# Kernel optimization log

Hardware: AMD Instinct MI355X
Metric: run time of the kernel (lower is better)

The kernel has to match this reference:

```python
import jax, jax.numpy as jnp
import numpy as np

EPS = 1e-5


def conv2d(x, w, b, pad):
    # x: [B,C,H,W], w: [O,I,kh,kw]
    out = jax.lax.conv_general_dilated(
        x, w, window_strides=(1, 1), padding=[(pad, pad), (pad, pad)],
        dimension_numbers=('NCHW', 'OIHW', 'NCHW'))
    return out + b[None, :, None, None]


def bilinear_gather(xf, py, px, H, W):
    # xf: [B,C,H*W]; py,px: [B,H,W] float sampling positions
    # zero padding outside the image (torchvision deform_conv2d semantics)
    y0 = jnp.floor(py)
    x0 = jnp.floor(px)
    wy = py - y0
    wx = px - x0
    y0i = y0.astype(jnp.int32)
    x0i = x0.astype(jnp.int32)
    B, C = xf.shape[0], xf.shape[1]
    acc = jnp.zeros((B, C, H, W), xf.dtype)
    for dy, wyv in ((0, 1.0 - wy), (1, wy)):
        for dx, wxv in ((0, 1.0 - wx), (1, wx)):
            yi = y0i + dy
            xi = x0i + dx
            valid = ((yi >= 0) & (yi < H) & (xi >= 0) & (xi < W)).astype(xf.dtype)
            idx = jnp.clip(yi, 0, H - 1) * W + jnp.clip(xi, 0, W - 1)  # [B,H,W]
            g = jnp.take_along_axis(xf, idx.reshape(B, 1, H * W), axis=2)
            g = g.reshape(B, C, H, W)
            acc = acc + g * (wyv * wxv * valid)[:, None]
    return acc


def deform_conv2d(x, offset, w, b, k):
    # x: [B,C,H,W]; offset: [B,2*k*k,H,W] ((dy,dx) pairs per kernel tap)
    B, C, H, W = x.shape
    pad = k // 2
    gy = jnp.arange(H, dtype=x.dtype)[None, :, None]
    gx = jnp.arange(W, dtype=x.dtype)[None, None, :]
    xf = x.reshape(B, C, H * W)
    out = jnp.zeros((B, w.shape[0], H, W), x.dtype)
    for i in range(k):
        for j in range(k):
            kk = i * k + j
            py = gy + (i - pad) + offset[:, 2 * kk]
            px = gx + (j - pad) + offset[:, 2 * kk + 1]
            samp = bilinear_gather(xf, py, px, H, W)  # [B,C,H,W]
            out = out + jnp.einsum('bchw,oc->bohw', samp, w[:, :, i, j])
    return out + b[None, :, None, None]


def setup_inputs() -> dict:
    key = jax.random.key(0)
    ks = jax.random.split(key, 16)
    B, C, H, W = 4, 64, 192, 192
    k = 3
    hid = max(1, C // 16)
    d = {}
    d['x'] = jax.random.normal(ks[0], (B, C, H, W), jnp.float32)
    # offset-prediction conv (3x3, pad 1) -> 2*k*k channels
    d['off_w'] = jax.random.normal(ks[1], (2 * k * k, C, 3, 3), jnp.float32) * 0.02
    d['off_b'] = jax.random.normal(ks[2], (2 * k * k,), jnp.float32) * 0.02
    # deformable conv weights (C->C, kxk)
    d['dw'] = jax.random.normal(ks[3], (C, C, k, k), jnp.float32) * 0.05
    d['db'] = jax.random.normal(ks[4], (C,), jnp.float32) * 0.05
    # BatchNorm (eval: running stats)
    d['bn_gamma'] = jnp.ones((C,), jnp.float32) + 0.1 * jax.random.normal(ks[5], (C,), jnp.float32)
    d['bn_beta'] = 0.1 * jax.random.normal(ks[6], (C,), jnp.float32)
    d['bn_mean'] = 0.1 * jax.random.normal(ks[7], (C,), jnp.float32)
    d['bn_var'] = jnp.ones((C,), jnp.float32)
    # channel attention: 1x1 squeeze / excite
    d['ca_w1'] = jax.random.normal(ks[8], (hid, C, 1, 1), jnp.float32) * 0.1
    d['ca_b1'] = jnp.zeros((hid,), jnp.float32)
    d['ca_w2'] = jax.random.normal(ks[9], (C, hid, 1, 1), jnp.float32) * 0.1
    d['ca_b2'] = jnp.zeros((C,), jnp.float32)
    # spatial attention: 7x7 conv -> 1 channel
    d['sa_w'] = jax.random.normal(ks[10], (1, C, 7, 7), jnp.float32) * 0.02
    d['sa_b'] = jnp.zeros((1,), jnp.float32)
    return d


def reference(x, off_w, off_b, dw, db, bn_gamma, bn_beta, bn_mean, bn_var,
              ca_w1, ca_b1, ca_w2, ca_b2, sa_w, sa_b):
    k = 3
    # extract: DeformableConv2d + BatchNorm2d
    offset = conv2d(x, off_w, off_b, pad=1)
    h = deform_conv2d(x, offset, dw, db, k)
    inv = jax.lax.rsqrt(bn_var + EPS)
    h = (h - bn_mean[None, :, None, None]) * (bn_gamma * inv)[None, :, None, None] \
        + bn_beta[None, :, None, None]
    # channel attention
    pooled = jnp.mean(h, axis=(2, 3), keepdims=True)  # [B,C,1,1]
    cw = conv2d(pooled, ca_w1, ca_b1, pad=0)
    cw = jax.nn.relu(cw)
    cw = conv2d(cw, ca_w2, ca_b2, pad=0)
    cw = jax.nn.sigmoid(cw)
    h = h * cw
    # spatial attention (7x7 conv, pad 3)
    sw = jax.nn.sigmoid(conv2d(h, sa_w, sa_b, pad=3))  # [B,1,H,W]
    h = h * sw
    return h
```

## Files before the change

kernel.cpp:

```cpp
#include <hip/hip_runtime.h>
#include <hip/hip_fp16.h>

#define H_  192
#define W_  192
#define HW  36864
#define B_  4

typedef __attribute__((ext_vector_type(8))) short short8;
typedef __attribute__((ext_vector_type(4))) float f32x4;
typedef __attribute__((ext_vector_type(4))) unsigned int u32x4;
typedef unsigned short ushort_t;
typedef unsigned int uint_t;

__device__ __forceinline__ ushort_t f2h(float v) {
    __half h = __float2half(v);
    ushort_t s;
    __builtin_memcpy(&s, &h, 2);
    return s;
}
__device__ __forceinline__ float h2f(ushort_t s) {
    __half h;
    __builtin_memcpy(&h, &s, 2);
    return __half2float(h);
}
__device__ __forceinline__ __half2 u2h2(uint_t u) {
    __half2 h;
    __builtin_memcpy(&h, &u, 4);
    return h;
}
__device__ __forceinline__ uint_t h22u(__half2 h) {
    uint_t u;
    __builtin_memcpy(&u, &h, 4);
    return u;
}
__device__ __forceinline__ short8 zero8() {
    u32x4 z = {0u, 0u, 0u, 0u};
    return __builtin_bit_cast(short8, z);
}

__device__ __forceinline__ void glds16(const ushort_t* src, void* lds_base) {
    __builtin_amdgcn_global_load_lds(
        (const __attribute__((address_space(1))) void*)src,
        (__attribute__((address_space(3))) void*)lds_base, 16, 0, 0);
}

__global__ void prep_kernel(const float* __restrict__ dw, const float* __restrict__ db,
                            const float* __restrict__ g, const float* __restrict__ be,
                            const float* __restrict__ mu, const float* __restrict__ var,
                            const float* __restrict__ ow,
                            ushort_t* __restrict__ w_bf, ushort_t* __restrict__ w_off,
                            float* __restrict__ scale, float* __restrict__ shift) {
    int idx = blockIdx.x * 256 + threadIdx.x;
    if (idx < 36864) {
        int tap = idx >> 12, o = (idx >> 6) & 63, c = idx & 63;
        w_bf[idx] = f2h(dw[(o * 64 + c) * 9 + tap]);
    }
    int idx2 = idx - 36864;
    if (idx2 >= 0 && idx2 < 18432) {
        int tap = idx2 >> 11, o = (idx2 >> 6) & 31, c = idx2 & 63;
        w_off[idx2] = (o < 18) ? f2h(ow[(o * 64 + c) * 9 + tap]) : (ushort_t)0;
    }
    if (idx < 64) {
        float s = g[idx] * rsqrtf(var[idx] + 1e-5f);
        scale[idx] = s;
        shift[idx] = (db[idx] - mu[idx]) * s + be[idx];
    }
}

__global__ __launch_bounds__(256) void transpose_kernel(const float* __restrict__ x,
                                                        ushort_t* __restrict__ x_t) {
    __shared__ uint_t tlds[256 * 33];
    int tid = threadIdx.x;
    int b = blockIdx.x / 144;
    int p0 = (blockIdx.x % 144) * 256;
    ushort_t* ts = (ushort_t*)tlds;
    for (int c = 0; c < 64; ++c) {
        float v = x[((size_t)(b * 64 + c)) * HW + p0 + tid];
        ts[tid * 66 + c] = f2h(v);
    }
    __syncthreads();
#pragma unroll
    for (int j = 0; j < 8; ++j) {
        int chunk = j * 256 + tid;
        int pl = chunk >> 3, s = chunk & 7;
        int bd = pl * 33 + s * 4;
        u32x4 v = {tlds[bd], tlds[bd + 1], tlds[bd + 2], tlds[bd + 3]};
        ((u32x4*)x_t)[(size_t)(b * HW + p0) * 8 + chunk] = v;
    }
}

__device__ __forceinline__ u32x4 prd(const ushort_t* patch, int q, int slot) {
    return *(const u32x4*)((const char*)patch + q * 128 + ((slot ^ (q & 7)) << 4));
}

__device__ __forceinline__ bool corner_setup2(float ody, float odx,
                                              int ybase, int xbase, int ytop, int xleft,
                                              int* q, int* g, float* w) {
    float py = (float)ybase + ody;
    float px = (float)xbase + odx;
    float fy = floorf(py), fx = floorf(px);
    int y0 = (int)fy, x0 = (int)fx;
    float wy = py - fy, wx = px - fx;
    int y0c = min(max(y0, 0), H_ - 1), y1c = min(max(y0 + 1, 0), H_ - 1);
    int x0c = min(max(x0, 0), W_ - 1), x1c = min(max(x0 + 1, 0), W_ - 1);
    float vy0 = (y0 >= 0 && y0 < H_) ? 1.f : 0.f;
    float vy1 = (y0 + 1 >= 0 && y0 + 1 < H_) ? 1.f : 0.f;
    float vx0 = (x0 >= 0 && x0 < W_) ? 1.f : 0.f;
    float vx1 = (x0 + 1 >= 0 && x0 + 1 < W_) ? 1.f : 0.f;
    w[0] = (1.f - wy) * (1.f - wx) * vy0 * vx0;
    w[1] = (1.f - wy) * wx * vy0 * vx1;
    w[2] = wy * (1.f - wx) * vy1 * vx0;
    w[3] = wy * wx * vy1 * vx1;
    g[0] = (y0c * W_ + x0c) * 64; g[1] = (y0c * W_ + x1c) * 64;
    g[2] = (y1c * W_ + x0c) * 64; g[3] = (y1c * W_ + x1c) * 64;
    int iy0 = y0c - ytop, iy1 = y1c - ytop;
    int ix0 = x0c - xleft, ix1 = x1c - xleft;
    q[0] = iy0 * 56 + ix0; q[1] = iy0 * 56 + ix1;
    q[2] = iy1 * 56 + ix0; q[3] = iy1 * 56 + ix1;
    return ((unsigned)iy0 <= 11u) & ((unsigned)iy1 <= 11u) &
           ((unsigned)ix0 <= 55u) & ((unsigned)ix1 <= 55u);
}

__device__ __forceinline__ short8 interp_f16(const u32x4* buf, const __half2* w2) {
    short8 r;
#pragma unroll
    for (int q = 0; q < 4; ++q) {
        __half2 acc = __hmul2(u2h2(buf[0][q]), w2[0]);
        acc = __hfma2(u2h2(buf[1][q]), w2[1], acc);
        acc = __hfma2(u2h2(buf[2][q]), w2[2], acc);
        acc = __hfma2(u2h2(buf[3][q]), w2[3], acc);
        ((uint_t*)&r)[q] = h22u(acc);
    }
    return r;
}

__global__ __launch_bounds__(576, 2) void deform_fused_kernel(
    const ushort_t* __restrict__ x_t, const ushort_t* __restrict__ w_off,
    const float* __restrict__ ob, const ushort_t* __restrict__ w_bf,
    const float* __restrict__ scale_g, const float* __restrict__ shift_g,
    float* __restrict__ out) {
    __shared__ __align__(16) ushort_t patch[672 * 64];

    int tid = threadIdx.x;
    int lane = tid & 63, w = tid >> 6;
    int tile = (blockIdx.x & 7) * 64 + (blockIdx.x >> 3);
    int b = tile / 128;
    int rem = tile % 128;
    int y0 = (rem >> 2) * 6;
    int x0 = (rem & 3) * 48;
    int ytop = y0 - 3, xleft = x0 - 4;

    int ln = lane & 15, kg = lane >> 4;
    int locA = w * 32 + ln, locB = locA + 16;
    int rowA = locA / 48, colA = locA - rowA * 48;
    int rowB = locB / 48, colB = locB - rowB * 48;
    int yA = y0 + rowA, xA = x0 + colA;
    int yB = y0 + rowB, xB = x0 + colB;
    const ushort_t* xt_b = x_t + (size_t)b * (HW * 64);

    {
        char* pbase = (char*)patch;
#pragma unroll
        for (int t = 0; t < 10; ++t) {
            if (t * 576 + w * 64 < 5376) {
                int g = t * 576 + tid;
                int q = g >> 3, sp = g & 7;
                int i = q / 56, j = q - i * 56;
                int pr = min(max(ytop + i, 0), H_ - 1);
                int pc = min(max(xleft + j, 0), W_ - 1);
                int s = sp ^ (q & 7);
                glds16(xt_b + (pr * W_ + pc) * 64 + s * 8,
                       pbase + (size_t)(t * 576 + w * 64) * 16);
            }
        }
    }
    asm volatile("s_waitcnt vmcnt(0)" ::: "memory");
    __syncthreads();

    f32x4 ao[2][2];
#pragma unroll
    for (int i = 0; i < 2; ++i)
#pragma unroll
        for (int j = 0; j < 2; ++j) ao[i][j] = (f32x4){0.f, 0.f, 0.f, 0.f};

    for (int tap = 0; tap < 9; ++tap) {
        int ti = tap / 3 - 1, tj = tap % 3 - 1;
        bool vA = ((unsigned)(yA + ti) < (unsigned)H_) && ((unsigned)(xA + tj) < (unsigned)W_);
        bool vB = ((unsigned)(yB + ti) < (unsigned)H_) && ((unsigned)(xB + tj) < (unsigned)W_);
        int qA = (rowA + 3 + ti) * 56 + (colA + 4 + tj);
        int qB = (rowB + 3 + ti) * 56 + (colB + 4 + tj);
        const ushort_t* wt = w_off + tap * 2048;
#pragma unroll
        for (int ks = 0; ks < 2; ++ks) {
            int ch = ks * 32 + kg * 8;
            int slot = kg + ks * 4;
            short8 a0 = *(const short8*)(wt + ln * 64 + ch);
            short8 a1 = *(const short8*)(wt + (16 + ln) * 64 + ch);
            short8 bA = vA ? __builtin_bit_cast(short8, prd(patch, qA, slot)) : zero8();
            short8 bB = vB ? __builtin_bit_cast(short8, prd(patch, qB, slot)) : zero8();
            ao[0][0] = __builtin_amdgcn_mfma_f32_16x16x32_f16(a0, bA, ao[0][0], 0, 0, 0);
            ao[0][1] = __builtin_amdgcn_mfma_f32_16x16x32_f16(a0, bB, ao[0][1], 0, 0, 0);
            ao[1][0] = __builtin_amdgcn_mfma_f32_16x16x32_f16(a1, bA, ao[1][0], 0, 0, 0);
            ao[1][1] = __builtin_amdgcn_mfma_f32_16x16x32_f16(a1, bB, ao[1][1], 0, 0, 0);
        }
    }

    float offA[18], offB[18];
#pragma unroll
    for (int m = 0; m < 18; ++m) {
        int src = (((m >> 2) & 3) << 4) | ln;
        float bias = ob[m];
        offA[m] = __shfl(ao[m >> 4][0][m & 3], src, 64) + bias;
        offB[m] = __shfl(ao[m >> 4][1][m & 3], src, 64) + bias;
    }

    f32x4 acc[4][2];
#pragma unroll
    for (int mt = 0; mt < 4; ++mt)
#pragma unroll
        for (int nt = 0; nt < 2; ++nt) acc[mt][nt] = (f32x4){0.f, 0.f, 0.f, 0.f};

#pragma unroll
    for (int tap = 0; tap < 9; ++tap) {
        int ti = tap / 3 - 1, tj = tap % 3 - 1;
        int qA[4], qB[4], gA[4], gB[4];
        float wA[4], wB[4];
        bool inA = corner_setup2(offA[2 * tap], offA[2 * tap + 1],
                                 yA + ti, xA + tj, ytop, xleft, qA, gA, wA);
        bool inB = corner_setup2(offB[2 * tap], offB[2 * tap + 1],
                                 yB + ti, xB + tj, ytop, xleft, qB, gB, wB);
        __half2 wA2[4], wB2[4];
#pragma unroll
        for (int c = 0; c < 4; ++c) {
            wA2[c] = __float2half2_rn(wA[c]);
            wB2[c] = __float2half2_rn(wB[c]);
        }
        const ushort_t* wt = w_bf + tap * 4096;
#pragma unroll
        for (int ks = 0; ks < 2; ++ks) {
            int ch = ks * 32 + kg * 8;
            int slot = kg + ks * 4;
            u32x4 cA[4], cB[4];
            if (__builtin_expect(inA, 1)) {
#pragma unroll
                for (int c = 0; c < 4; ++c) cA[c] = prd(patch, qA[c], slot);
            } else {
#pragma unroll
                for (int c = 0; c < 4; ++c) cA[c] = *(const u32x4*)(xt_b + gA[c] + ch);
            }
            if (__builtin_expect(inB, 1)) {
#pragma unroll
                for (int c = 0; c < 4; ++c) cB[c] = prd(patch, qB[c], slot);
            } else {
#pragma unroll
                for (int c = 0; c < 4; ++c) cB[c] = *(const u32x4*)(xt_b + gB[c] + ch);
            }
            short8 fA = interp_f16(cA, wA2);
            short8 fB = interp_f16(cB, wB2);
            short8 a0 = *(const short8*)(wt + (0 + ln) * 64 + ch);
            short8 a1 = *(const short8*)(wt + (16 + ln) * 64 + ch);
            short8 a2 = *(const short8*)(wt + (32 + ln) * 64 + ch);
            short8 a3 = *(const short8*)(wt + (48 + ln) * 64 + ch);
            acc[0][0] = __builtin_amdgcn_mfma_f32_16x16x32_f16(a0, fA, acc[0][0], 0, 0, 0);
            acc[0][1] = __builtin_amdgcn_mfma_f32_16x16x32_f16(a0, fB, acc[0][1], 0, 0, 0);
            acc[1][0] = __builtin_amdgcn_mfma_f32_16x16x32_f16(a1, fA, acc[1][0], 0, 0, 0);
            acc[1][1] = __builtin_amdgcn_mfma_f32_16x16x32_f16(a1, fB, acc[1][1], 0, 0, 0);
            acc[2][0] = __builtin_amdgcn_mfma_f32_16x16x32_f16(a2, fA, acc[2][0], 0, 0, 0);
            acc[2][1] = __builtin_amdgcn_mfma_f32_16x16x32_f16(a2, fB, acc[2][1], 0, 0, 0);
            acc[3][0] = __builtin_amdgcn_mfma_f32_16x16x32_f16(a3, fA, acc[3][0], 0, 0, 0);
            acc[3][1] = __builtin_amdgcn_mfma_f32_16x16x32_f16(a3, fB, acc[3][1], 0, 0, 0);
        }
    }

    int pixA = yA * W_ + xA;
    int pixB = yB * W_ + xB;
#pragma unroll
    for (int mt = 0; mt < 4; ++mt) {
#pragma unroll
        for (int r = 0; r < 4; ++r) {
            int m = mt * 16 + kg * 4 + r;
            float sc = scale_g[m], sh = shift_g[m];
            size_t obase = (size_t)(b * 64 + m) * HW;
            out[obase + pixA] = acc[mt][0][r] * sc + sh;
            out[obase + pixB] = acc[mt][1][r] * sc + sh;
        }
    }
}

__global__ __launch_bounds__(256) void pool_kernel(const float* __restrict__ h,
                                                   float* __restrict__ pooled) {
    __shared__ float red[4];
    int tid = threadIdx.x;
    const float* src = h + (size_t)blockIdx.x * HW;
    float s = 0.f;
#pragma unroll 4
    for (int i = tid * 4; i < HW; i += 1024) {
        float4 v = *(const float4*)(src + i);
        s += v.x + v.y + v.z + v.w;
    }
#pragma unroll
    for (int d = 1; d < 64; d <<= 1) s += __shfl_xor(s, d, 64);
    if ((tid & 63) == 0) red[tid >> 6] = s;
    __syncthreads();
    if (tid == 0)
        pooled[blockIdx.x] = (red[0] + red[1] + red[2] + red[3]) * (1.0f / (float)HW);
}

__global__ void ca_kernel(const float* __restrict__ pooled_g,
                          const float* __restrict__ w1, const float* __restrict__ b1,
                          const float* __restrict__ w2, const float* __restrict__ b2,
                          const float* __restrict__ saw, float* __restrict__ cw,
                          ushort_t* __restrict__ we_bf) {
    __shared__ float pooled[256];
    __shared__ float t1[16];
    int t = threadIdx.x;
    int b = t >> 6, o = t & 63;
    pooled[t] = pooled_g[t];
    __syncthreads();
    if (t < 16) {
        int bb = t >> 2, hh = t & 3;
        float a = b1[hh];
        for (int c = 0; c < 64; ++c) a += pooled[bb * 64 + c] * w1[hh * 64 + c];
        t1[t] = fmaxf(a, 0.f);
    }
    __syncthreads();
    float a = b2[o];
#pragma unroll
    for (int h2 = 0; h2 < 4; ++h2) a += t1[b * 4 + h2] * w2[o * 4 + h2];
    float cwv = 1.f / (1.f + __expf(-a));
    cw[t] = cwv;
    for (int tap = 0; tap < 64; ++tap) {
        float v = (tap < 49) ? cwv * saw[o * 49 + tap] : 0.f;
        we_bf[(b * 64 + tap) * 64 + o] = f2h(v);
    }
}

__global__ __launch_bounds__(256) void tap_gemm_kernel(
    const float* __restrict__ h, const ushort_t* __restrict__ we_bf,
    ushort_t* __restrict__ u) {
    int tid = threadIdx.x;
    int b = blockIdx.y;
    int p0 = blockIdx.x * 128;
    int wid = tid >> 6, lane = tid & 63, ln = lane & 15, kg = lane >> 4;
    int pA = p0 + wid * 32 + ln, pB = pA + 16;
    const float* hb = h + (size_t)b * 64 * HW;
    const ushort_t* wt = we_bf + b * 4096;

    f32x4 acc[4][2];
#pragma unroll
    for (int mt = 0; mt < 4; ++mt)
#pragma unroll
        for (int nt = 0; nt < 2; ++nt) acc[mt][nt] = (f32x4){0.f, 0.f, 0.f, 0.f};

#pragma unroll
    for (int ks = 0; ks < 2; ++ks) {
        int ch = ks * 32 + kg * 8;
        short8 fA, fB;
#pragma unroll
        for (int q = 0; q < 8; ++q) {
            fA[q] = (short)f2h(hb[(size_t)(ch + q) * HW + pA]);
            fB[q] = (short)f2h(hb[(size_t)(ch + q) * HW + pB]);
        }
        short8 a0 = *(const short8*)(wt + (0 + ln) * 64 + ch);
        short8 a1 = *(const short8*)(wt + (16 + ln) * 64 + ch);
        short8 a2 = *(const short8*)(wt + (32 + ln) * 64 + ch);
        short8 a3 = *(const short8*)(wt + (48 + ln) * 64 + ch);
        acc[0][0] = __builtin_amdgcn_mfma_f32_16x16x32_f16(a0, fA, acc[0][0], 0, 0, 0);
        acc[0][1] = __builtin_amdgcn_mfma_f32_16x16x32_f16(a0, fB, acc[0][1], 0, 0, 0);
        acc[1][0] = __builtin_amdgcn_mfma_f32_16x16x32_f16(a1, fA, acc[1][0], 0, 0, 0);
        acc[1][1] = __builtin_amdgcn_mfma_f32_16x16x32_f16(a1, fB, acc[1][1], 0, 0, 0);
        acc[2][0] = __builtin_amdgcn_mfma_f32_16x16x32_f16(a2, fA, acc[2][0], 0, 0, 0);
        acc[2][1] = __builtin_amdgcn_mfma_f32_16x16x32_f16(a2, fB, acc[2][1], 0, 0, 0);
        acc[3][0] = __builtin_amdgcn_mfma_f32_16x16x32_f16(a3, fA, acc[3][0], 0, 0, 0);
        acc[3][1] = __builtin_amdgcn_mfma_f32_16x16x32_f16(a3, fB, acc[3][1], 0, 0, 0);
    }
#pragma unroll
    for (int mt = 0; mt < 4; ++mt)
#pragma unroll
        for (int r = 0; r < 4; ++r) {
            int m = mt * 16 + kg * 4 + r;
            if (m < 49) {
                ushort_t* up = u + (size_t)(b * 49 + m) * HW;
                up[pA] = f2h(acc[mt][0][r]);
                up[pB] = f2h(acc[mt][1][r]);
            }
        }
}

__global__ __launch_bounds__(256) void sa_final_kernel(
    float* __restrict__ out, const ushort_t* __restrict__ u,
    const float* __restrict__ cw, const float* __restrict__ sab) {
    __shared__ float cw_l[64];
    int tid = threadIdx.x;
    int b = blockIdx.y;
    int p = blockIdx.x * 256 + tid;
    if (tid < 64) cw_l[tid] = cw[b * 64 + tid];
    __syncthreads();
    int y = p / 192, x = p - y * 192;
    float s = sab[0];
    const ushort_t* ub = u + (size_t)b * 49 * HW;
#pragma unroll
    for (int dy = 0; dy < 7; ++dy)
#pragma unroll
        for (int dx = 0; dx < 7; ++dx) {
            int yy = y + dy - 3, xx = x + dx - 3;
            bool ok = ((unsigned)yy < 192u) && ((unsigned)xx < 192u);
            int ad = ok ? (p + (dy - 3) * 192 + (dx - 3)) : 0;
            float v = h2f(ub[(size_t)(dy * 7 + dx) * HW + ad]);
            s += ok ? v : 0.f;
        }
    float swv = 1.f / (1.f + __expf(-s));
#pragma unroll 8
    for (int c = 0; c < 64; ++c) {
        size_t ix = (size_t)(b * 64 + c) * HW + p;
        out[ix] = out[ix] * (cw_l[c] * swv);
    }
}

extern "C" void kernel_launch(void* const* d_in, const int* in_sizes, int n_in,
                              void* d_out, int out_size, void* d_ws, size_t ws_size,
                              hipStream_t stream) {
    const float* x     = (const float*)d_in[0];
    const float* off_w = (const float*)d_in[1];
    const float* off_b = (const float*)d_in[2];
    const float* dw    = (const float*)d_in[3];
    const float* db    = (const float*)d_in[4];
    const float* bn_g  = (const float*)d_in[5];
    const float* bn_b  = (const float*)d_in[6];
    const float* bn_m  = (const float*)d_in[7];
    const float* bn_v  = (const float*)d_in[8];
    const float* ca_w1 = (const float*)d_in[9];
    const float* ca_b1 = (const float*)d_in[10];
    const float* ca_w2 = (const float*)d_in[11];
    const float* ca_b2 = (const float*)d_in[12];
    const float* sa_w  = (const float*)d_in[13];
    const float* sa_b  = (const float*)d_in[14];
    float* out = (float*)d_out;
    float* ws  = (float*)d_ws;

    ushort_t* x_t    = (ushort_t*)ws;
    ushort_t* u      = (ushort_t*)ws;
    ushort_t* w_bf   = (ushort_t*)(ws + 4718592);
    ushort_t* w_off  = (ushort_t*)(ws + 4737024);
    ushort_t* we_bf  = (ushort_t*)(ws + 4737024);
    float* scale     = ws + 4746240;
    float* shift     = ws + 4746304;
    float* cw        = ws + 4746368;
    float* pooled    = ws + 4746624;

    prep_kernel<<<216, 256, 0, stream>>>(dw, db, bn_g, bn_b, bn_m, bn_v, off_w,
                                         w_bf, w_off, scale, shift);
    transpose_kernel<<<576, 256, 0, stream>>>(x, x_t);
    deform_fused_kernel<<<512, 576, 0, stream>>>(x_t, w_off, off_b, w_bf,
                                                 scale, shift, out);
    pool_kernel<<<256, 256, 0, stream>>>(out, pooled);
    ca_kernel<<<1, 256, 0, stream>>>(pooled, ca_w1, ca_b1, ca_w2, ca_b2, sa_w, cw, we_bf);
    tap_gemm_kernel<<<dim3(288, 4), 256, 0, stream>>>(out, we_bf, u);
    sa_final_kernel<<<dim3(144, 4), 256, 0, stream>>>(out, u, cw, sa_b);
}
```

Before: 134.1 us.

## Fuse channel mean pooling into deform conv epilogue with per-tile partial sums

The deform conv epilogue now reduces each output channel's values per tile through shuffles and shared memory, and writes per-tile partial sums. A small reduce kernel replaces the pool kernel that re-read the full 37 MB output. This removes one full pass over the output at the cost of extra epilogue work and two block syncs. The launch bound's minimum blocks per CU also drops from 2 to 1, which may allow more registers but could lower occupancy.

```diff
diff --git a/kernel.cpp b/kernel.cpp
--- a/kernel.cpp
+++ b/kernel.cpp
@@ -134,11 +134,11 @@
     return r;
 }
 
-__global__ __launch_bounds__(576, 2) void deform_fused_kernel(
+__global__ __launch_bounds__(576, 1) void deform_fused_kernel(
     const ushort_t* __restrict__ x_t, const ushort_t* __restrict__ w_off,
     const float* __restrict__ ob, const ushort_t* __restrict__ w_bf,
     const float* __restrict__ scale_g, const float* __restrict__ shift_g,
-    float* __restrict__ out) {
+    float* __restrict__ out, float* __restrict__ partial) {
     __shared__ __align__(16) ushort_t patch[672 * 64];
 
     int tid = threadIdx.x;
@@ -274,6 +274,7 @@
 
     int pixA = yA * W_ + xA;
     int pixB = yB * W_ + xB;
+    float vsum[4][4];
 #pragma unroll
     for (int mt = 0; mt < 4; ++mt) {
 #pragma unroll
@@ -281,29 +282,47 @@
             int m = mt * 16 + kg * 4 + r;
             float sc = scale_g[m], sh = shift_g[m];
             size_t obase = (size_t)(b * 64 + m) * HW;
-            out[obase + pixA] = acc[mt][0][r] * sc + sh;
-            out[obase + pixB] = acc[mt][1][r] * sc + sh;
-        }
-    }
-}
-
-__global__ __launch_bounds__(256) void pool_kernel(const float* __restrict__ h,
-                                                   float* __restrict__ pooled) {
-    __shared__ float red[4];
-    int tid = threadIdx.x;
-    const float* src = h + (size_t)blockIdx.x * HW;
+            float v0 = acc[mt][0][r] * sc + sh;
+            float v1 = acc[mt][1][r] * sc + sh;
+            out[obase + pixA] = v0;
+            out[obase + pixB] = v1;
+            vsum[mt][r] = v0 + v1;
+        }
+    }
+
+    __syncthreads();
+    float* red = (float*)patch;
+#pragma unroll
+    for (int mt = 0; mt < 4; ++mt)
+#pragma unroll
+        for (int r = 0; r < 4; ++r) {
+            int m = mt * 16 + kg * 4 + r;
+            float vs = vsum[mt][r];
+            vs += __shfl_xor(vs, 1, 16);
+            vs += __shfl_xor(vs, 2, 16);
+            vs += __shfl_xor(vs, 4, 16);
+            vs += __shfl_xor(vs, 8, 16);
+            if (ln == 0) red[m * 9 + w] = vs;
+        }
+    __syncthreads();
+    if (tid < 64) {
+        float s = 0.f;
+#pragma unroll
+        for (int q = 0; q < 9; ++q) s += red[tid * 9 + q];
+        partial[tid * 512 + tile] = s;
+    }
+}
+
+__global__ __launch_bounds__(64) void reduce_kernel(const float* __restrict__ partial,
+                                                    float* __restrict__ pooled) {
+    int o = blockIdx.x & 63, b = blockIdx.x >> 6;
+    const float* pr = partial + o * 512 + b * 128;
+    int t = threadIdx.x;
     float s = 0.f;
-#pragma unroll 4
-    for (int i = tid * 4; i < HW; i += 1024) {
-        float4 v = *(const float4*)(src + i);
-        s += v.x + v.y + v.z + v.w;
-    }
+    for (int q = t; q < 128; q += 64) s += pr[q];
 #pragma unroll
     for (int d = 1; d < 64; d <<= 1) s += __shfl_xor(s, d, 64);
-    if ((tid & 63) == 0) red[tid >> 6] = s;
-    __syncthreads();
-    if (tid == 0)
-        pooled[blockIdx.x] = (red[0] + red[1] + red[2] + red[3]) * (1.0f / (float)HW);
+    if (t == 0) pooled[b * 64 + o] = s * (1.0f / (float)HW);
 }
 
 __global__ void ca_kernel(const float* __restrict__ pooled_g,
@@ -447,13 +466,14 @@
     float* shift     = ws + 4746304;
     float* cw        = ws + 4746368;
     float* pooled    = ws + 4746624;
+    float* partial   = ws + 4746880;
 
     prep_kernel<<<216, 256, 0, stream>>>(dw, db, bn_g, bn_b, bn_m, bn_v, off_w,
                                          w_bf, w_off, scale, shift);
     transpose_kernel<<<576, 256, 0, stream>>>(x, x_t);
     deform_fused_kernel<<<512, 576, 0, stream>>>(x_t, w_off, off_b, w_bf,
-                                                 scale, shift, out);
-    pool_kernel<<<256, 256, 0, stream>>>(out, pooled);
+                                                 scale, shift, out, partial);
+    reduce_kernel<<<256, 64, 0, stream>>>(partial, pooled);
     ca_kernel<<<1, 256, 0, stream>>>(pooled, ca_w1, ca_b1, ca_w2, ca_b2, sa_w, cw, we_bf);
     tap_gemm_kernel<<<dim3(288, 4), 256, 0, stream>>>(out, we_bf, u);
     sa_final_kernel<<<dim3(144, 4), 256, 0, stream>>>(out, u, cw, sa_b);
```

Result: no change. 136.0 us (+1.4%).

## Store intermediate activations as fp16, fuse pooling partials, merge prep and transpose

Applied to the files above, without the earlier changes.

The deform kernel now writes the BN-applied activation as fp16 into a workspace buffer instead of fp32 into the output. It also emits per-wave channel partial sums, which a tiny reduce kernel combines, replacing the full-tensor pool pass. The prep and transpose kernels are merged into one launch, and the later tap-GEMM and final kernels read the fp16 intermediate. This cuts global memory traffic and launch count. The cost is fp16 rounding of the intermediate and a larger workspace requirement, with a fallback path when the workspace is too small.

```diff
diff --git a/kernel.cpp b/kernel.cpp
--- a/kernel.cpp
+++ b/kernel.cpp
@@ -44,13 +44,18 @@
         (__attribute__((address_space(3))) void*)lds_base, 16, 0, 0);
 }
 
-__global__ void prep_kernel(const float* __restrict__ dw, const float* __restrict__ db,
-                            const float* __restrict__ g, const float* __restrict__ be,
-                            const float* __restrict__ mu, const float* __restrict__ var,
-                            const float* __restrict__ ow,
-                            ushort_t* __restrict__ w_bf, ushort_t* __restrict__ w_off,
-                            float* __restrict__ scale, float* __restrict__ shift) {
-    int idx = blockIdx.x * 256 + threadIdx.x;
+__global__ __launch_bounds__(256) void prep_transpose_kernel(
+    const float* __restrict__ x, ushort_t* __restrict__ x_t,
+    const float* __restrict__ dw, const float* __restrict__ db,
+    const float* __restrict__ g, const float* __restrict__ be,
+    const float* __restrict__ mu, const float* __restrict__ var,
+    const float* __restrict__ ow,
+    ushort_t* __restrict__ w_bf, ushort_t* __restrict__ w_off,
+    float* __restrict__ scale, float* __restrict__ shift) {
+    __shared__ uint_t tlds[256 * 33];
+    int tid = threadIdx.x;
+
+    int idx = blockIdx.x * 256 + tid;
     if (idx < 36864) {
         int tap = idx >> 12, o = (idx >> 6) & 63, c = idx & 63;
         w_bf[idx] = f2h(dw[(o * 64 + c) * 9 + tap]);
@@ -65,12 +70,7 @@
         scale[idx] = s;
         shift[idx] = (db[idx] - mu[idx]) * s + be[idx];
     }
-}
-
-__global__ __launch_bounds__(256) void transpose_kernel(const float* __restrict__ x,
-                                                        ushort_t* __restrict__ x_t) {
-    __shared__ uint_t tlds[256 * 33];
-    int tid = threadIdx.x;
+
     int b = blockIdx.x / 144;
     int p0 = (blockIdx.x % 144) * 256;
     ushort_t* ts = (ushort_t*)tlds;
@@ -134,11 +134,12 @@
     return r;
 }
 
+template <bool POOL>
 __global__ __launch_bounds__(576, 2) void deform_fused_kernel(
     const ushort_t* __restrict__ x_t, const ushort_t* __restrict__ w_off,
     const float* __restrict__ ob, const ushort_t* __restrict__ w_bf,
     const float* __restrict__ scale_g, const float* __restrict__ shift_g,
-    float* __restrict__ out) {
+    ushort_t* __restrict__ h16, float* __restrict__ partial) {
     __shared__ __align__(16) ushort_t patch[672 * 64];
 
     int tid = threadIdx.x;
@@ -274,6 +275,7 @@
 
     int pixA = yA * W_ + xA;
     int pixB = yB * W_ + xB;
+    float vsum[4][4];
 #pragma unroll
     for (int mt = 0; mt < 4; ++mt) {
 #pragma unroll
@@ -281,22 +283,64 @@
             int m = mt * 16 + kg * 4 + r;
             float sc = scale_g[m], sh = shift_g[m];
             size_t obase = (size_t)(b * 64 + m) * HW;
-            out[obase + pixA] = acc[mt][0][r] * sc + sh;
-            out[obase + pixB] = acc[mt][1][r] * sc + sh;
-        }
-    }
-}
-
-__global__ __launch_bounds__(256) void pool_kernel(const float* __restrict__ h,
+            float v0 = acc[mt][0][r] * sc + sh;
+            float v1 = acc[mt][1][r] * sc + sh;
+            h16[obase + pixA] = f2h(v0);
+            h16[obase + pixB] = f2h(v1);
+            vsum[mt][r] = v0 + v1;
+        }
+    }
+
+    if constexpr (POOL) {
+        float vs[4][4];
+#pragma unroll
+        for (int mt = 0; mt < 4; ++mt)
+#pragma unroll
+            for (int r = 0; r < 4; ++r) {
+                float v = vsum[mt][r];
+                v += __shfl_xor(v, 1, 16);
+                v += __shfl_xor(v, 2, 16);
+                v += __shfl_xor(v, 4, 16);
+                v += __shfl_xor(v, 8, 16);
+                vs[mt][r] = v;
+            }
+        int rl = lane & 3, ml = (lane >> 2) & 3;
+        float val = vs[0][0];
+#pragma unroll
+        for (int mt = 0; mt < 4; ++mt)
+#pragma unroll
+            for (int r = 0; r < 4; ++r)
+                val = (ml == mt && rl == r) ? vs[mt][r] : val;
+        int c = kg * 4 + rl + 16 * ml;
+        partial[(size_t)(tile * 9 + w) * 64 + c] = val;
+    }
+}
+
+__global__ __launch_bounds__(256) void reduce_kernel(const float* __restrict__ partial,
+                                                     float* __restrict__ pooled) {
+    __shared__ float red[256];
+    int b = blockIdx.x, t = threadIdx.x, c = t & 63, qq = t >> 6;
+    float s = 0.f;
+    for (int row = qq * 288; row < qq * 288 + 288; ++row)
+        s += partial[(size_t)(b * 1152 + row) * 64 + c];
+    red[t] = s;
+    __syncthreads();
+    if (t < 64)
+        pooled[b * 64 + t] = (red[t] + red[t + 64] + red[t + 128] + red[t + 192]) *
+                             (1.0f / (float)HW);
+}
+
+__global__ __launch_bounds__(256) void pool_kernel(const ushort_t* __restrict__ h,
                                                    float* __restrict__ pooled) {
     __shared__ float red[4];
     int tid = threadIdx.x;
-    const float* src = h + (size_t)blockIdx.x * HW;
+    const ushort_t* src = h + (size_t)blockIdx.x * HW;
     float s = 0.f;
-#pragma unroll 4
-    for (int i = tid * 4; i < HW; i += 1024) {
-        float4 v = *(const float4*)(src + i);
-        s += v.x + v.y + v.z + v.w;
+#pragma unroll 2
+    for (int i = tid * 8; i < HW; i += 2048) {
+        short8 v = *(const short8*)(src + i);
+#pragma unroll
+        for (int q = 0; q < 8; ++q) s += h2f((ushort_t)v[q]);
     }
 #pragma unroll
     for (int d = 1; d < 64; d <<= 1) s += __shfl_xor(s, d, 64);
@@ -336,14 +380,14 @@
 }
 
 __global__ __launch_bounds__(256) void tap_gemm_kernel(
-    const float* __restrict__ h, const ushort_t* __restrict__ we_bf,
+    const ushort_t* __restrict__ h, const ushort_t* __restrict__ we_bf,
     ushort_t* __restrict__ u) {
     int tid = threadIdx.x;
     int b = blockIdx.y;
     int p0 = blockIdx.x * 128;
     int wid = tid >> 6, lane = tid & 63, ln = lane & 15, kg = lane >> 4;
     int pA = p0 + wid * 32 + ln, pB = pA + 16;
-    const float* hb = h + (size_t)b * 64 * HW;
+    const ushort_t* hb = h + (size_t)b * 64 * HW;
     const ushort_t* wt = we_bf + b * 4096;
 
     f32x4 acc[4][2];
@@ -358,8 +402,8 @@
         short8 fA, fB;
 #pragma unroll
         for (int q = 0; q < 8; ++q) {
-            fA[q] = (short)f2h(hb[(size_t)(ch + q) * HW + pA]);
-            fB[q] = (short)f2h(hb[(size_t)(ch + q) * HW + pB]);
+            fA[q] = (short)hb[(size_t)(ch + q) * HW + pA];
+            fB[q] = (short)hb[(size_t)(ch + q) * HW + pB];
         }
         short8 a0 = *(const short8*)(wt + (0 + ln) * 64 + ch);
         short8 a1 = *(const short8*)(wt + (16 + ln) * 64 + ch);
@@ -388,7 +432,8 @@
 }
 
 __global__ __launch_bounds__(256) void sa_final_kernel(
-    float* __restrict__ out, const ushort_t* __restrict__ u,
+    float* __restrict__ out, const ushort_t* __restrict__ h,
+    const ushort_t* __restrict__ u,
     const float* __restrict__ cw, const float* __restrict__ sab) {
     __shared__ float cw_l[64];
     int tid = threadIdx.x;
@@ -413,7 +458,7 @@
 #pragma unroll 8
     for (int c = 0; c < 64; ++c) {
         size_t ix = (size_t)(b * 64 + c) * HW + p;
-        out[ix] = out[ix] * (cw_l[c] * swv);
+        out[ix] = h2f(h[ix]) * (cw_l[c] * swv);
     }
 }
 
@@ -440,21 +485,30 @@
 
     ushort_t* x_t    = (ushort_t*)ws;
     ushort_t* u      = (ushort_t*)ws;
-    ushort_t* w_bf   = (ushort_t*)(ws + 4718592);
-    ushort_t* w_off  = (ushort_t*)(ws + 4737024);
-    ushort_t* we_bf  = (ushort_t*)(ws + 4737024);
-    float* scale     = ws + 4746240;
-    float* shift     = ws + 4746304;
-    float* cw        = ws + 4746368;
-    float* pooled    = ws + 4746624;
-
-    prep_kernel<<<216, 256, 0, stream>>>(dw, db, bn_g, bn_b, bn_m, bn_v, off_w,
-                                         w_bf, w_off, scale, shift);
-    transpose_kernel<<<576, 256, 0, stream>>>(x, x_t);
-    deform_fused_kernel<<<512, 576, 0, stream>>>(x_t, w_off, off_b, w_bf,
-                                                 scale, shift, out);
-    pool_kernel<<<256, 256, 0, stream>>>(out, pooled);
+    ushort_t* h16    = (ushort_t*)(ws + 4718592);
+    ushort_t* w_bf   = (ushort_t*)(ws + 9437184);
+    ushort_t* w_off  = (ushort_t*)(ws + 9455616);
+    ushort_t* we_bf  = (ushort_t*)(ws + 9455616);
+    float* scale     = ws + 9464832;
+    float* shift     = ws + 9464896;
+    float* cw        = ws + 9464960;
+    float* pooled    = ws + 9465216;
+    float* partial   = ws + 9465472;
+
+    const size_t NEED_A2 = 9760384ull * 4ull;
+
+    prep_transpose_kernel<<<576, 256, 0, stream>>>(x, x_t, dw, db, bn_g, bn_b, bn_m,
+                                                   bn_v, off_w, w_bf, w_off, scale, shift);
+    if (ws_size >= NEED_A2) {
+        deform_fused_kernel<true><<<512, 576, 0, stream>>>(x_t, w_off, off_b, w_bf,
+                                                           scale, shift, h16, partial);
+        reduce_kernel<<<4, 256, 0, stream>>>(partial, pooled);
+    } else {
+        deform_fused_kernel<false><<<512, 576, 0, stream>>>(x_t, w_off, off_b, w_bf,
+                                                            scale, shift, h16, partial);
+        pool_kernel<<<256, 256, 0, stream>>>(h16, pooled);
+    }
     ca_kernel<<<1, 256, 0, stream>>>(pooled, ca_w1, ca_b1, ca_w2, ca_b2, sa_w, cw, we_bf);
-    tap_gemm_kernel<<<dim3(288, 4), 256, 0, stream>>>(out, we_bf, u);
-    sa_final_kernel<<<dim3(144, 4), 256, 0, stream>>>(out, u, cw, sa_b);
-}
+    tap_gemm_kernel<<<dim3(288, 4), 256, 0, stream>>>(h16, we_bf, u);
+    sa_final_kernel<<<dim3(144, 4), 256, 0, stream>>>(out, h16, u, cw, sa_b);
+}
```

New measurement: 129.6 us. -3.4%, faster.
